# Performance work log

Measured on AMD Instinct MI355X. Metric: run time of the kernel, lower is better.

## Reference

```python
import jax, jax.numpy as jnp
import numpy as np

M = 41
RHO = M / 2.0          # rho=-1 -> M/2
OVERLAPS = 40
STRIDES = 40
N_FFT = OVERLAPS + STRIDES   # 80
HOP = STRIDES                # 40

def _get_index():
    S = []
    for n1 in range(-(M // 2), M // 2):
        for n2 in range(-(M // 2), M // 2):
            if abs(n1 * n2) <= RHO * (M // 2):
                S.append((n1, n2))
    return np.asarray(S, dtype=np.int64)

IDX = _get_index()          # [K,2], K=1600
N1 = IDX[:, 0]
N2 = IDX[:, 1]
K = len(IDX)

def setup_inputs() -> dict:
    key = jax.random.key(0)
    ks = jax.random.split(key, 7)
    b, L, m = 2, 2080, 2
    return {
        "x_real": jax.random.normal(ks[0], (b, L, m), jnp.float32),
        "x_imag": jax.random.normal(ks[1], (b, L, m), jnp.float32),
        "task_info": jax.random.uniform(ks[2], (b, 4), jnp.float32),
        "w_real": jax.random.normal(ks[3], (K,), jnp.float32) * 0.02,
        "w_imag": jax.random.normal(ks[4], (K,), jnp.float32) * 0.02,
        "b_real": jax.random.normal(ks[5], (1,), jnp.float32) * 0.02,
        "b_imag": jax.random.normal(ks[6], (1,), jnp.float32) * 0.02,
    }

def _stft(x):
    # x: [b, L, m] complex -> [b, T, F, m]; rectangular window, center=False
    L = x.shape[1]
    T = (L - N_FFT) // HOP + 1
    idx = np.arange(T)[:, None] * HOP + np.arange(N_FFT)[None, :]
    frames = x[:, idx, :]                      # [b, T, F, m]
    return jnp.fft.fft(frames, axis=2)

def _istft(X, L):
    # X: [b, T, F, m] -> [b, L, m] via overlap-add, rect-window normalization
    frames = jnp.fft.ifft(X, axis=2)
    b, T, F, m = X.shape
    idx = (np.arange(T)[:, None] * HOP + np.arange(F)[None, :]).reshape(-1)
    y = jnp.zeros((b, L, m), X.dtype).at[:, idx, :].add(frames.reshape(b, -1, m))
    cov = np.zeros(L)
    np.add.at(cov, idx, 1.0)
    cov = jnp.asarray(np.where(cov > 0, cov, 1.0), jnp.float32)
    return y / cov[None, :, None]

def reference(x_real, x_imag, task_info, w_real, w_imag, b_real, b_imag):
    x = x_real + 1j * x_imag                   # [b, L, m] complex64
    b, L, m = x.shape
    # get_power: launch power (dBm in task_info[:,0]) -> mW per mode
    P = jnp.power(10.0, task_info[:, 0] / 10.0) / m   # [b]
    X = _stft(x)                               # [b, T, F, m]
    F = N_FFT
    f = np.arange(F)
    g1 = (f[None, :] - N1[:, None]) % F        # [K, F] : torch.roll(X, n1, dims=2)
    g12 = (f[None, :] - (N1 + N2)[:, None]) % F
    g2 = (f[None, :] - N2[:, None]) % F
    # A_k = roll(X,n1) * conj(roll(X,n1+n2))   -> [b, T, K, F, m]
    A = X[:, :, g1, :] * jnp.conj(X[:, :, g12, :])
    A = A + jnp.roll(A, 1, axis=1)             # + previous frame (circular)
    E = A * X[:, :, g2, :]                     # [b, T, K, F, m]
    w = (w_real + 1j * w_imag).astype(E.dtype)
    bias = (b_real[0] + 1j * b_imag[0]).astype(E.dtype)
    delta = jnp.einsum('btkfm,k->btfm', E, w) + bias   # ComplexLinear(K,1)
    d = _istft(delta, L)                       # [b, L, m]
    out = x + d * P[:, None, None].astype(d.dtype)
    return out[:, OVERLAPS // 2: L - OVERLAPS // 2, :]
```

## Files before the change

### kernel.cpp

```cpp
#include <hip/hip_runtime.h>
#include <math.h>

#define BATCH 2
#define LLEN  2080
#define MCH   2
#define TT    51
#define FF    80
#define HOP   40
#define KW    1600
#define OUTL  2040
#define NT    640
#define PI_F  3.14159265358979323846f

__global__ __launch_bounds__(NT) void fused_kernel(
    const float* __restrict__ xr, const float* __restrict__ xi,
    const float* __restrict__ wr, const float* __restrict__ wi,
    const float* __restrict__ br, const float* __restrict__ bi,
    float2* __restrict__ Fr)
{
    __shared__ float2 xs[2 * FF];
    __shared__ float2 tw[FF];
    __shared__ float2 Yt2[2 * FF];
    __shared__ float2 Yp[FF];
    __shared__ float2 Wsh[KW];
    __shared__ float2 Zall[40][2 * FF];
    __shared__ float2 dvec[FF];

    float2* red  = &Zall[0][0];
    float2 (*redD)[FF] = (float2(*)[FF])&Zall[0][0];

    int tid = threadIdx.x;
    int bid = blockIdx.x;
    int b   = bid / (TT * MCH);
    int rem = bid % (TT * MCH);
    int t   = rem / MCH;
    int mi  = rem % MCH;
    int tp  = (t + TT - 1) % TT;

    if (tid < FF) {
        int g = (b * LLEN + t * HOP + tid) * MCH + mi;
        xs[tid] = make_float2(xr[g], xi[g]);
        float s, c;
        sincosf((2.0f * PI_F / FF) * (float)tid, &s, &c);
        tw[tid] = make_float2(c, s);
    } else if (tid < 2 * FF) {
        int j = tid - FF;
        int g = (b * LLEN + tp * HOP + j) * MCH + mi;
        xs[tid] = make_float2(xr[g], xi[g]);
    } else {
        for (int k = tid - 2 * FF; k < KW; k += NT - 2 * FF)
            Wsh[k] = make_float2(wr[k], wi[k]);
    }
    __syncthreads();

    {
        int o    = tid >> 2;
        int part = tid & 3;
        int ff   = o % FF;
        int frm  = o / FF;
        const float2* xb = &xs[frm * FF];
        float2 a = make_float2(0.f, 0.f);
        int j0 = part * 20;
        int r  = (ff * j0) % FF;
        for (int j = j0; j < j0 + 20; ++j) {
            float2 xv = xb[j];
            float2 tv = tw[r];
            a.x += xv.x * tv.x + xv.y * tv.y;
            a.y += xv.y * tv.x - xv.x * tv.y;
            r += ff; if (r >= FF) r -= FF;
        }
        red[part * 160 + o] = a;
    }
    __syncthreads();
    if (tid < 2 * FF) {
        float2 s = make_float2(0.f, 0.f);
        for (int p = 0; p < 4; ++p) {
            float2 v = red[p * 160 + tid];
            s.x += v.x; s.y += v.y;
        }
        if (tid < FF) {
            Yt2[tid + 20] = s;
            Yt2[(tid < 60) ? (tid + 100) : (tid - 60)] = s;
        } else {
            Yp[tid - FF] = s;
        }
    }
    __syncthreads();

    for (int i = 0; i < 5; ++i) {
        int zi = tid + i * NT;
        int jn = zi / FF;
        int g  = zi % FF;
        int n2 = jn - 20;
        int gm = g - n2; if (gm >= FF) gm -= FF; if (gm < 0) gm += FF;
        float2 a  = Yt2[g + 20], bm = Yt2[gm + 20];
        float2 cc = Yp[g],       dm = Yp[gm];
        float zre = a.x * bm.x + a.y * bm.y + cc.x * dm.x + cc.y * dm.y;
        float zim = a.y * bm.x - a.x * bm.y + cc.y * dm.x - cc.x * dm.y;
        float2 z = make_float2(zre, zim);
        Zall[jn][g + 20] = z;
        Zall[jn][(g < 60) ? (g + 100) : (g - 60)] = z;
    }
    __syncthreads();

    float2 o0, o1, o2, o3, o4;
    int jn, fb;
    {
        jn = tid >> 4;
        int fg = tid & 15;
        fb = fg * 5;
        const float2* zz = Zall[jn];

        float2 S0 = make_float2(0.f,0.f), S1 = S0, S2 = S0, S3 = S0, S4 = S0;
        float2 w0 = zz[fb + 40], w1 = zz[fb + 41], w2 = zz[fb + 42],
               w3 = zz[fb + 43], w4 = zz[fb + 44];
        #pragma unroll
        for (int jn1 = 0; jn1 < 40; ++jn1) {
            float2 wv = Wsh[jn1 * 40 + jn];
            S0.x += wv.x * w0.x - wv.y * w0.y;  S0.y += wv.x * w0.y + wv.y * w0.x;
            S1.x += wv.x * w1.x - wv.y * w1.y;  S1.y += wv.x * w1.y + wv.y * w1.x;
            S2.x += wv.x * w2.x - wv.y * w2.y;  S2.y += wv.x * w2.y + wv.y * w2.x;
            S3.x += wv.x * w3.x - wv.y * w3.y;  S3.y += wv.x * w3.y + wv.y * w3.x;
            S4.x += wv.x * w4.x - wv.y * w4.y;  S4.y += wv.x * w4.y + wv.y * w4.x;
            if (jn1 < 39) {
                float2 nv = zz[fb + 39 - jn1];
                w4 = w3; w3 = w2; w2 = w1; w1 = w0; w0 = nv;
            }
        }
        float2 y;
        y = Yt2[fb + 0 - jn + 40]; o0 = make_float2(y.x*S0.x - y.y*S0.y, y.x*S0.y + y.y*S0.x);
        y = Yt2[fb + 1 - jn + 40]; o1 = make_float2(y.x*S1.x - y.y*S1.y, y.x*S1.y + y.y*S1.x);
        y = Yt2[fb + 2 - jn + 40]; o2 = make_float2(y.x*S2.x - y.y*S2.y, y.x*S2.y + y.y*S2.x);
        y = Yt2[fb + 3 - jn + 40]; o3 = make_float2(y.x*S3.x - y.y*S3.y, y.x*S3.y + y.y*S3.x);
        y = Yt2[fb + 4 - jn + 40]; o4 = make_float2(y.x*S4.x - y.y*S4.y, y.x*S4.y + y.y*S4.x);
    }
    __syncthreads();
    redD[jn][fb + 0] = o0;
    redD[jn][fb + 1] = o1;
    redD[jn][fb + 2] = o2;
    redD[jn][fb + 3] = o3;
    redD[jn][fb + 4] = o4;
    __syncthreads();
    if (tid < FF) {
        float2 s = make_float2(br[0], bi[0]);
        for (int p = 0; p < 40; ++p) {
            float2 v = redD[p][tid];
            s.x += v.x; s.y += v.y;
        }
        dvec[tid] = s;
    }
    __syncthreads();

    {
        int j    = tid >> 3;
        int part = tid & 7;
        float2 a = make_float2(0.f, 0.f);
        int f0 = part * 10;
        int r  = (j * f0) % FF;
        for (int ff2 = f0; ff2 < f0 + 10; ++ff2) {
            float2 dv = dvec[ff2];
            float2 tv = tw[r];
            a.x += dv.x * tv.x - dv.y * tv.y;
            a.y += dv.x * tv.y + dv.y * tv.x;
            r += j; if (r >= FF) r -= FF;
        }
        red[part * FF + j] = a;
    }
    __syncthreads();
    if (tid < FF) {
        float2 s = make_float2(0.f, 0.f);
        for (int p = 0; p < 8; ++p) {
            float2 v = red[p * FF + tid];
            s.x += v.x; s.y += v.y;
        }
        s.x *= (1.0f / FF);
        s.y *= (1.0f / FF);
        Fr[((b * TT + t) * MCH + mi) * FF + tid] = s;
    }
}

__global__ void out_kernel(
    const float* __restrict__ xr, const float* __restrict__ xi,
    const float* __restrict__ ti, const float2* __restrict__ Fr,
    float* __restrict__ out, int out_size)
{
    int idx = blockIdx.x * blockDim.x + threadIdx.x;
    int tot = BATCH * OUTL * MCH;
    if (idx >= tot) return;
    int mi  = idx % MCH;
    int rem = idx / MCH;
    int lo  = rem % OUTL;
    int b   = rem / OUTL;
    int l   = lo + 20;

    float P = exp2f(ti[b * 4] * 0.33219280948873623f) * 0.5f;

    int t1 = l / HOP;
    int t0 = t1 - 1;
    float2 acc = make_float2(0.f, 0.f);
    float cov = 0.f;
    if (t1 <= TT - 1) {
        float2 v = Fr[((b * TT + t1) * MCH + mi) * FF + (l - HOP * t1)];
        acc.x += v.x; acc.y += v.y; cov += 1.f;
    }
    if (t0 >= 0) {
        float2 v = Fr[((b * TT + t0) * MCH + mi) * FF + (l - HOP * t0)];
        acc.x += v.x; acc.y += v.y; cov += 1.f;
    }
    float inv = 1.0f / cov;
    acc.x *= inv; acc.y *= inv;

    int gi = (b * LLEN + l) * MCH + mi;
    float outr = xr[gi] + acc.x * P;
    if (out_size == tot) {
        out[idx] = outr;
    } else {
        float outi = xi[gi] + acc.y * P;
        out[idx * 2]     = outr;
        out[idx * 2 + 1] = outi;
    }
}

extern "C" void kernel_launch(void* const* d_in, const int* in_sizes, int n_in,
                              void* d_out, int out_size, void* d_ws, size_t ws_size,
                              hipStream_t stream)
{
    const float* xr = (const float*)d_in[0];
    const float* xi = (const float*)d_in[1];
    const float* ti = (const float*)d_in[2];
    const float* wr = (const float*)d_in[3];
    const float* wi = (const float*)d_in[4];
    const float* br = (const float*)d_in[5];
    const float* bi = (const float*)d_in[6];

    float2* Fr = (float2*)d_ws;

    int nb = BATCH * TT * MCH;
    fused_kernel<<<nb, NT, 0, stream>>>(xr, xi, wr, wi, br, bi, Fr);

    int tot = BATCH * OUTL * MCH;
    out_kernel<<<(tot + 255) / 256, 256, 0, stream>>>(xr, xi, ti, Fr,
                                                      (float*)d_out, out_size);
}
```

Measured before the change: 16.96 us.

## Prefetch weights to registers, recurrence twiddles, pad Zall, two-level reduction

Several local changes land together in the fused kernel. The weight loads are issued into registers at kernel start and written to shared memory later, so their latency overlaps the DFT stage. The forward DFT now builds twiddles by complex rotation from a starting quarter-turn value instead of indexed table lookups. Zall rows are padded to 161 entries to change the bank mapping, and the 40-way delta reduction is split into two levels so all threads take part. The rotation recurrence can add small floating-point rounding error.

```diff
diff --git a/kernel.cpp b/kernel.cpp
--- a/kernel.cpp
+++ b/kernel.cpp
@@ -10,9 +10,11 @@
 #define KW    1600
 #define OUTL  2040
 #define NT    640
+#define NB    (BATCH * TT * MCH)
+#define ZROW  161
 #define PI_F  3.14159265358979323846f
 
-__global__ __launch_bounds__(NT) void fused_kernel(
+__global__ __launch_bounds__(NT) void fused_k1(
     const float* __restrict__ xr, const float* __restrict__ xi,
     const float* __restrict__ wr, const float* __restrict__ wi,
     const float* __restrict__ br, const float* __restrict__ bi,
@@ -23,11 +25,10 @@
     __shared__ float2 Yt2[2 * FF];
     __shared__ float2 Yp[FF];
     __shared__ float2 Wsh[KW];
-    __shared__ float2 Zall[40][2 * FF];
+    __shared__ float2 Zall[40][ZROW];
     __shared__ float2 dvec[FF];
 
-    float2* red  = &Zall[0][0];
-    float2 (*redD)[FF] = (float2(*)[FF])&Zall[0][0];
+    float2* flat = &Zall[0][0];
 
     int tid = threadIdx.x;
     int bid = blockIdx.x;
@@ -37,45 +38,61 @@
     int mi  = rem % MCH;
     int tp  = (t + TT - 1) % TT;
 
-    if (tid < FF) {
-        int g = (b * LLEN + t * HOP + tid) * MCH + mi;
+    float bre = br[0], bim = bi[0];
+
+    float2 wreg0 = make_float2(wr[tid],        wi[tid]);
+    float2 wreg1 = make_float2(wr[tid + NT],   wi[tid + NT]);
+    float2 wreg2 = make_float2(0.f, 0.f);
+    if (tid < KW - 2 * NT)
+        wreg2 = make_float2(wr[tid + 2 * NT], wi[tid + 2 * NT]);
+
+    if (tid < 2 * FF) {
+        int frm = tid / FF, j = tid % FF;
+        int tt  = (frm == 0) ? t : tp;
+        int g = (b * LLEN + tt * HOP + j) * MCH + mi;
         xs[tid] = make_float2(xr[g], xi[g]);
+    } else if (tid < 240) {
+        int jj = tid - 160;
         float s, c;
-        sincosf((2.0f * PI_F / FF) * (float)tid, &s, &c);
-        tw[tid] = make_float2(c, s);
-    } else if (tid < 2 * FF) {
-        int j = tid - FF;
-        int g = (b * LLEN + tp * HOP + j) * MCH + mi;
-        xs[tid] = make_float2(xr[g], xi[g]);
-    } else {
-        for (int k = tid - 2 * FF; k < KW; k += NT - 2 * FF)
-            Wsh[k] = make_float2(wr[k], wi[k]);
+        sincosf((2.0f * PI_F / FF) * (float)jj, &s, &c);
+        tw[jj] = make_float2(c, s);
     }
     __syncthreads();
 
     {
         int o    = tid >> 2;
-        int part = tid & 3;
+        int pq   = tid & 3;
         int ff   = o % FF;
         int frm  = o / FF;
         const float2* xb = &xs[frm * FF];
+
+        int q = (ff * pq) & 3;
+        float2 tv = (q == 0) ? make_float2(1.f, 0.f)
+                  : (q == 1) ? make_float2(0.f, -1.f)
+                  : (q == 2) ? make_float2(-1.f, 0.f)
+                  :            make_float2(0.f, 1.f);
+        float sp, cp;
+        sincosf(-(2.0f * PI_F / FF) * (float)ff, &sp, &cp);
+        float2 st = make_float2(cp, sp);
+
         float2 a = make_float2(0.f, 0.f);
-        int j0 = part * 20;
-        int r  = (ff * j0) % FF;
-        for (int j = j0; j < j0 + 20; ++j) {
+        int j = pq * 20;
+        #pragma unroll 4
+        for (int i = 0; i < 20; ++i, ++j) {
             float2 xv = xb[j];
-            float2 tv = tw[r];
-            a.x += xv.x * tv.x + xv.y * tv.y;
-            a.y += xv.y * tv.x - xv.x * tv.y;
-            r += ff; if (r >= FF) r -= FF;
-        }
-        red[part * 160 + o] = a;
+            a.x += xv.x * tv.x - xv.y * tv.y;
+            a.y += xv.x * tv.y + xv.y * tv.x;
+            float nx = tv.x * st.x - tv.y * st.y;
+            tv.y = tv.x * st.y + tv.y * st.x;
+            tv.x = nx;
+        }
+        flat[pq * 160 + o] = a;
     }
     __syncthreads();
     if (tid < 2 * FF) {
         float2 s = make_float2(0.f, 0.f);
         for (int p = 0; p < 4; ++p) {
-            float2 v = red[p * 160 + tid];
+            float2 v = flat[p * 160 + tid];
             s.x += v.x; s.y += v.y;
         }
         if (tid < FF) {
@@ -101,6 +118,11 @@
         Zall[jn][g + 20] = z;
         Zall[jn][(g < 60) ? (g + 100) : (g - 60)] = z;
     }
+    {
+        Wsh[tid]      = wreg0;
+        Wsh[tid + NT] = wreg1;
+        if (tid < KW - 2 * NT) Wsh[tid + 2 * NT] = wreg2;
+    }
     __syncthreads();
 
     float2 o0, o1, o2, o3, o4;
@@ -109,7 +131,7 @@
         jn = tid >> 4;
         int fg = tid & 15;
         fb = fg * 5;
-        const float2* zz = Zall[jn];
+        const float2* zz = &Zall[jn][0];
 
         float2 S0 = make_float2(0.f,0.f), S1 = S0, S2 = S0, S3 = S0, S4 = S0;
         float2 w0 = zz[fb + 40], w1 = zz[fb + 41], w2 = zz[fb + 42],
@@ -135,16 +157,29 @@
         y = Yt2[fb + 4 - jn + 40]; o4 = make_float2(y.x*S4.x - y.y*S4.y, y.x*S4.y + y.y*S4.x);
     }
     __syncthreads();
-    redD[jn][fb + 0] = o0;
-    redD[jn][fb + 1] = o1;
-    redD[jn][fb + 2] = o2;
-    redD[jn][fb + 3] = o3;
-    redD[jn][fb + 4] = o4;
+    flat[jn * FF + fb + 0] = o0;
+    flat[jn * FF + fb + 1] = o1;
+    flat[jn * FF + fb + 2] = o2;
+    flat[jn * FF + fb + 3] = o3;
+    flat[jn * FF + fb + 4] = o4;
+    __syncthreads();
+
+    {
+        int f = tid % FF;
+        int p = tid / FF;
+        float2 s = make_float2(0.f, 0.f);
+        for (int q2 = 0; q2 < 5; ++q2) {
+            float2 v = flat[(p * 5 + q2) * FF + f];
+            s.x += v.x; s.y += v.y;
+        }
+        flat[3200 + p * FF + f] = s;
+    }
     __syncthreads();
     if (tid < FF) {
-        float2 s = make_float2(br[0], bi[0]);
-        for (int p = 0; p < 40; ++p) {
-            float2 v = redD[p][tid];
+        float2 s = make_float2(bre, bim);
+        #pragma unroll
+        for (int p = 0; p < 8; ++p) {
+            float2 v = flat[3200 + p * FF + tid];
             s.x += v.x; s.y += v.y;
         }
         dvec[tid] = s;
@@ -152,25 +187,27 @@
     __syncthreads();
 
     {
-        int j    = tid >> 3;
-        int part = tid & 7;
+        int j  = tid >> 3;
+        int p8 = tid & 7;
         float2 a = make_float2(0.f, 0.f);
-        int f0 = part * 10;
+        int f0 = p8 * 10;
         int r  = (j * f0) % FF;
-        for (int ff2 = f0; ff2 < f0 + 10; ++ff2) {
-            float2 dv = dvec[ff2];
+        #pragma unroll 5
+        for (int i = 0; i < 10; ++i) {
+            float2 dv = dvec[f0 + i];
             float2 tv = tw[r];
             a.x += dv.x * tv.x - dv.y * tv.y;
             a.y += dv.x * tv.y + dv.y * tv.x;
             r += j; if (r >= FF) r -= FF;
         }
-        red[part * FF + j] = a;
+        flat[p8 * FF + j] = a;
     }
     __syncthreads();
     if (tid < FF) {
         float2 s = make_float2(0.f, 0.f);
+        #pragma unroll
         for (int p = 0; p < 8; ++p) {
-            float2 v = red[p * FF + tid];
+            float2 v = flat[p * FF + tid];
             s.x += v.x; s.y += v.y;
         }
         s.x *= (1.0f / FF);
@@ -235,8 +272,7 @@
 
     float2* Fr = (float2*)d_ws;
 
-    int nb = BATCH * TT * MCH;
-    fused_kernel<<<nb, NT, 0, stream>>>(xr, xi, wr, wi, br, bi, Fr);
+    fused_k1<<<NB, NT, 0, stream>>>(xr, xi, wr, wi, br, bi, Fr);
 
     int tot = BATCH * OUTL * MCH;
     out_kernel<<<(tot + 255) / 256, 256, 0, stream>>>(xr, xi, ti, Fr,
```

New measurement: 17.22 us. No clear change (+1.6%).
